# Optimization experiments

Hardware: AMD Instinct MI355X
Metric: run time of the kernel (lower is better)

Reference implementation:

```python
import jax, jax.numpy as jnp
import numpy as np
import math

D_MODEL = 2048
D_STATE = 64
D_CONV = 4
EXPAND = 2
HEADDIM = 128
NGROUPS = 1
CHUNK = 256
D_INNER = EXPAND * D_MODEL            # 4096
NHEADS = D_INNER // HEADDIM           # 32
CONV_DIM = D_INNER + 2 * NGROUPS * D_STATE   # 4224
D_IN_PROJ = 2 * D_INNER + 2 * NGROUPS * D_STATE + NHEADS  # 8352
BATCH, SEQLEN = 2, 4096
EPS = 1e-5


def segsum(x):
    # x: (..., T) -> (..., T, T) with s[i, j] = sum_{k=j+1}^{i} x[k], -inf above diag
    T = x.shape[-1]
    xx = jnp.broadcast_to(x[..., :, None], x.shape + (T,))
    mask_lo = jnp.tril(jnp.ones((T, T), dtype=bool), -1)
    xx = jnp.where(mask_lo, xx, 0.0)
    s = jnp.cumsum(xx, axis=-2)
    mask = jnp.tril(jnp.ones((T, T), dtype=bool), 0)
    return jnp.where(mask, s, -jnp.inf)


def ssd(X, A, B, C, block_len):
    # X:(b,L,h,p)  A:(b,L,h)  B,C:(b,L,h,n)
    b, L, h, p = X.shape
    c = L // block_len
    X = X.reshape(b, c, block_len, h, p)
    A = A.reshape(b, c, block_len, h).transpose(0, 3, 1, 2)  # b h c l
    B = B.reshape(b, c, block_len, h, -1)
    C = C.reshape(b, c, block_len, h, -1)
    A_cumsum = jnp.cumsum(A, axis=-1)
    Lmat = jnp.exp(segsum(A))                                  # b h c l l
    Y_diag = jnp.einsum('bclhn,bcshn,bhcls,bcshp->bclhp', C, B, Lmat, X)
    decay_states = jnp.exp(A_cumsum[:, :, :, -1:] - A_cumsum)  # b h c l
    states = jnp.einsum('bclhn,bhcl,bclhp->bchpn', B, decay_states, X)
    init = jnp.zeros_like(states[:, :1])
    states = jnp.concatenate([init, states], axis=1)
    decay_chunk = jnp.exp(segsum(jnp.pad(A_cumsum[:, :, :, -1], ((0, 0), (0, 0), (1, 0)))))
    new_states = jnp.einsum('bhzc,bchpn->bzhpn', decay_chunk, states)
    states, final_state = new_states[:, :-1], new_states[:, -1]
    Y_off = jnp.einsum('bclhn,bchpn,bhcl->bclhp', C, states, jnp.exp(A_cumsum))
    Y = (Y_diag + Y_off).reshape(b, L, h, p)
    return Y, final_state


def causal_dwconv(x, w, b):
    # x:(B,L,C)  w:(C,K) depthwise kernel  b:(C,)  -> causal conv, length preserved
    C, K = w.shape
    y = jax.lax.conv_general_dilated(
        x.transpose(0, 2, 1), w[:, None, :], (1,), [(K - 1, 0)],
        feature_group_count=C)
    return y.transpose(0, 2, 1) + b


def setup_inputs() -> dict:
    key = jax.random.key(0)
    ks = jax.random.split(key, 8)
    u = jax.random.normal(ks[0], (BATCH, SEQLEN, D_MODEL), dtype=jnp.float32)
    W_in = jax.random.normal(ks[1], (D_MODEL, D_IN_PROJ), dtype=jnp.float32) / np.sqrt(D_MODEL)
    conv_w = jax.random.normal(ks[2], (CONV_DIM, D_CONV), dtype=jnp.float32) / np.sqrt(D_CONV)
    conv_b = jnp.zeros((CONV_DIM,), dtype=jnp.float32)
    # dt_bias init: inverse-softplus of dt sampled log-uniform in [dt_min, dt_max]
    dt_min, dt_max, dt_floor = 1e-3, 1e-1, 1e-4
    dt = jnp.exp(jax.random.uniform(ks[3], (NHEADS,)) * (math.log(dt_max) - math.log(dt_min)) + math.log(dt_min))
    dt = jnp.clip(dt, dt_floor)
    dt_bias = dt + jnp.log(-jnp.expm1(-dt))
    A_log = jnp.log(jax.random.uniform(ks[4], (NHEADS,), minval=1.0, maxval=16.0))
    D = jnp.ones((NHEADS,), dtype=jnp.float32)
    norm_w = jnp.ones((D_INNER,), dtype=jnp.float32)
    W_out = jax.random.normal(ks[5], (D_INNER, D_MODEL), dtype=jnp.float32) / np.sqrt(D_INNER)
    return {"u": u, "W_in": W_in, "conv_w": conv_w, "conv_b": conv_b,
            "dt_bias": dt_bias, "A_log": A_log, "D": D, "norm_w": norm_w, "W_out": W_out}


def reference(u, W_in, conv_w, conv_b, dt_bias, A_log, D, norm_w, W_out):
    batch, seqlen, _ = u.shape
    zxbcdt = u @ W_in                                   # (B,L,8352)
    z, xBC, dt = jnp.split(zxbcdt, [D_INNER, D_INNER + CONV_DIM], axis=-1)
    dt = jax.nn.softplus(dt + dt_bias)                  # (B,L,H)
    xBC = jax.nn.silu(causal_dwconv(xBC, conv_w, conv_b))
    x, B, C = jnp.split(xBC, [D_INNER, D_INNER + NGROUPS * D_STATE], axis=-1)
    x = x.reshape(batch, seqlen, NHEADS, HEADDIM)
    B = jnp.broadcast_to(B.reshape(batch, seqlen, NGROUPS, D_STATE), (batch, seqlen, NHEADS, D_STATE))
    C = jnp.broadcast_to(C.reshape(batch, seqlen, NGROUPS, D_STATE), (batch, seqlen, NHEADS, D_STATE))
    A = -jnp.exp(A_log)                                 # (H,)
    x_scaled = x * dt[..., None]
    A_dt = A * dt                                       # (B,L,H)
    y, _final = ssd(x_scaled, A_dt, B, C, CHUNK)
    y = y.reshape(batch, seqlen, D_INNER)
    x_flat = x.reshape(batch, seqlen, D_INNER)
    D_full = jnp.repeat(D, HEADDIM)
    y = y + x_flat * D_full
    # gated RMSNorm, norm AFTER gate (norm_before_gate=False)
    yg = y * jax.nn.silu(z)
    var = jnp.mean(yg * yg, axis=-1, keepdims=True)
    y = yg * jax.lax.rsqrt(var + EPS) * norm_w
    return y @ W_out
```

## Files before the change

### kernel.cpp

```cpp
#include <hip/hip_runtime.h>

typedef short s8v __attribute__((ext_vector_type(8)));
typedef float f4v __attribute__((ext_vector_type(4)));
typedef unsigned short bfu;

#define MFMA16 __builtin_amdgcn_mfma_f32_16x16x32_bf16

constexpr int kSEQ = 4096;
constexpr int kBL  = 8192;
constexpr int kDM  = 2048;
constexpr int kDP  = 8352;
constexpr int kDPpad = 8448;
constexpr int kDI  = 4096;
constexpr int kCV  = 4224;
constexpr int kXBC = 4256;
constexpr int kNH  = 32;
constexpr int kHD  = 128;
constexpr int kDS  = 64;
constexpr int kCH  = 256;

#if defined(__has_builtin)
#  if __has_builtin(__builtin_amdgcn_global_load_lds)
#    define HAS_GLD 1
#  endif
#endif
#ifndef HAS_GLD
#  define HAS_GLD 0
#endif

__device__ __forceinline__ void gld_lds16(const void* g, void* lbase, int lane){
#if HAS_GLD
  (void)lane;
  __builtin_amdgcn_global_load_lds(
      (const __attribute__((address_space(1))) void*)g,
      (__attribute__((address_space(3))) void*)lbase, 16, 0, 0);
#else
  *(uint4*)((char*)lbase + lane * 16) = *(const uint4*)g;
#endif
}

__device__ __forceinline__ bfu f2bf(float f){
  union { float f; unsigned u; } c; c.f = f;
  return (bfu)((c.u + 0x7fffu + ((c.u >> 16) & 1u)) >> 16);
}
__device__ __forceinline__ float bf2f(bfu s){
  union { unsigned u; float f; } c; c.u = ((unsigned)s) << 16;
  return c.f;
}

__device__ __forceinline__ s8v frag_ld(const char* lds, int rowbase, int kh, int lane){
  int r = rowbase + (lane & 15);
  int slot = (kh << 2) + (lane >> 4);
  return *(const s8v*)(lds + (((r << 3) + (slot ^ (r & 7))) << 4));
}

__global__ __launch_bounds__(256) void k_zero(bfu* __restrict__ p, int n){
  int i = blockIdx.x * 256 + threadIdx.x;
  if (i < n) p[i] = 0;
}

__global__ __launch_bounds__(256) void k_cvt(const float* __restrict__ s, bfu* __restrict__ d, int n8){
  int i = blockIdx.x * 256 + threadIdx.x;
  int stride = gridDim.x * 256;
  for (; i < n8; i += stride){
    const float4* sp = (const float4*)(s + (size_t)i * 8);
    float4 a = sp[0], b = sp[1];
    uint4 pk; bfu* pp = (bfu*)&pk;
    pp[0]=f2bf(a.x); pp[1]=f2bf(a.y); pp[2]=f2bf(a.z); pp[3]=f2bf(a.w);
    pp[4]=f2bf(b.x); pp[5]=f2bf(b.y); pp[6]=f2bf(b.z); pp[7]=f2bf(b.w);
    *(uint4*)(d + (size_t)i * 8) = pk;
  }
}

__global__ __launch_bounds__(256) void k_transpose(const float* __restrict__ src, bfu* __restrict__ dst,
                                                   int R, int C, const float* __restrict__ scale){
  __shared__ float tile[32][33];
  int c0 = blockIdx.x * 32, r0 = blockIdx.y * 32;
  int tx = threadIdx.x, ty = threadIdx.y;
  #pragma unroll
  for (int i = ty; i < 32; i += 8){
    int r = r0 + i, cc = c0 + tx;
    tile[i][tx] = (r < R && cc < C) ? src[(size_t)r * C + cc] : 0.f;
  }
  __syncthreads();
  #pragma unroll
  for (int i = ty; i < 32; i += 8){
    int dr = c0 + i, dc = r0 + tx;
    if (dr < C && dc < R){
      float v = tile[tx][i];
      if (scale) v *= scale[dc];
      dst[(size_t)dr * R + dc] = f2bf(v);
    }
  }
}

template<int MODE>
__global__ __launch_bounds__(512, 2) void k_gemm256(const bfu* __restrict__ A, const bfu* __restrict__ Bt,
                                                    float* __restrict__ outF, bfu* __restrict__ outZ,
                                                    bfu* __restrict__ outX, const float* __restrict__ rsv,
                                                    int tilesN, int N, int K){
  extern __shared__ char lds[];
  int t = threadIdx.x, lane = t & 63, wave = t >> 6;
  int wr = wave >> 2, wc = wave & 3;
  int nwg = gridDim.x;
  int bid = blockIdx.x;
  int cpx = nwg >> 3;
  int wg = (bid & 7) * cpx + (bid >> 3);
  int tmTile = wg / tilesN, tnTile = wg % tilesN;
  int tm = tmTile << 8, tn = tnTile << 8;
  const bfu* Ab = A + (size_t)tm * K;
  const bfu* Bb = Bt + (size_t)tn * K;

  #define AU(b,kh) ((b) * 65536 + (kh) * 16384)
  #define BU(b,kh) ((b) * 65536 + 32768 + (kh) * 16384)

  auto stage_unit = [&](const bfu* srcbase, int unitOfs, int kcol0){
    #pragma unroll
    for (int j = 0; j < 2; ++j){
      int lg = j * 512 + wave * 64 + lane;
      int r = lg >> 2;
      int s = (lg & 3) ^ ((r >> 1) & 3);
      gld_lds16(srcbase + (size_t)r * K + kcol0 + s * 8,
                lds + unitOfs + (j * 512 + wave * 64) * 16, lane);
    }
  };
  auto rd_frag = [&](int unitOfs, int rbase) -> s8v {
    int r = rbase + (lane & 15);
    int s = lane >> 4;
    int g = (r << 2) + (s ^ ((r >> 1) & 3));
    return *(const s8v*)(lds + unitOfs + (g << 4));
  };

  f4v acc[8][4];
  f4v zz = {0.f, 0.f, 0.f, 0.f};
  #pragma unroll
  for (int m = 0; m < 8; ++m)
    #pragma unroll
    for (int n = 0; n < 4; ++n) acc[m][n] = zz;

  int nt = K >> 6;
  stage_unit(Ab, AU(0,0), 0);
  stage_unit(Bb, BU(0,0), 0);
  stage_unit(Ab, AU(0,1), 32);
  stage_unit(Bb, BU(0,1), 32);
  __builtin_amdgcn_sched_barrier(0);
  asm volatile("s_waitcnt vmcnt(4)" ::: "memory");
  __builtin_amdgcn_sched_barrier(0);
  __builtin_amdgcn_s_barrier();
  __builtin_amdgcn_sched_barrier(0);

  #pragma unroll 1
  for (int tt = 0; tt < nt; ++tt){
    int cb = tt & 1, nb = cb ^ 1;
    int k0n = (tt + 1) << 6;
    bool more = (tt + 1 < nt);
    #pragma unroll
    for (int kh = 0; kh < 2; ++kh){
      if (more){
        stage_unit(Ab, AU(nb,kh), k0n + kh * 32);
        stage_unit(Bb, BU(nb,kh), k0n + kh * 32);
      }
      s8v af[8], bf[4];
      #pragma unroll
      for (int m = 0; m < 8; ++m) af[m] = rd_frag(AU(cb,kh), wr * 128 + m * 16);
      #pragma unroll
      for (int n = 0; n < 4; ++n) bf[n] = rd_frag(BU(cb,kh), wc * 64 + n * 16);
      __builtin_amdgcn_s_setprio(1);
      #pragma unroll
      for (int n = 0; n < 4; ++n)
        #pragma unroll
        for (int m = 0; m < 8; ++m)
          acc[m][n] = MFMA16(af[m], bf[n], acc[m][n], 0, 0, 0);
      __builtin_amdgcn_s_setprio(0);
      __builtin_amdgcn_sched_barrier(0);
      if (more) { asm volatile("s_waitcnt vmcnt(4)" ::: "memory"); }
      else      { asm volatile("s_waitcnt vmcnt(0)" ::: "memory"); }
      __builtin_amdgcn_sched_barrier(0);
      __builtin_amdgcn_s_barrier();
      __builtin_amdgcn_sched_barrier(0);
    }
  }

  int r0 = (lane >> 4) << 2;
  if (MODE == 0){
    float* rsl = (float*)lds;
    if (t < 256) rsl[t] = rsv[tm + t];
    __syncthreads();
    #pragma unroll
    for (int m = 0; m < 8; ++m)
      #pragma unroll
      for (int n = 0; n < 4; ++n)
        #pragma unroll
        for (int r = 0; r < 4; ++r){
          int rl = wr * 128 + m * 16 + r0 + r;
          size_t rg = (size_t)(tm + rl);
          int cg = tn + wc * 64 + n * 16 + (lane & 15);
          outF[rg * N + cg] = acc[m][n][r] * rsl[rl];
        }
  } else {
    #pragma unroll
    for (int m = 0; m < 8; ++m)
      #pragma unroll
      for (int n = 0; n < 4; ++n){
        int col = wc * 64 + n * 16 + (lane & 15);
        int cs = col >> 3, cl = col & 7;
        #pragma unroll
        for (int r = 0; r < 4; ++r){
          int row = wr * 128 + m * 16 + r0 + r;
          *(bfu*)(lds + row * 512 + ((cs ^ (row & 7)) << 4) + cl * 2) = f2bf(acc[m][n][r]);
        }
      }
    __syncthreads();
    bfu* op; int ldo, cofs;
    if (tn < 4096){ op = outZ; ldo = 4096; cofs = 0; }
    else          { op = outX; ldo = kXBC; cofs = 4096; }
    int row = t >> 1, half = t & 1;
    bfu* baseo = op + (size_t)(tm + row) * ldo + (tn - cofs) + half * 128;
    #pragma unroll
    for (int i = 0; i < 16; ++i){
      int cg = tn + half * 128 + i * 8;
      if (cg < kDP){
        uint4 v = *(const uint4*)(lds + row * 512 + (((half * 16 + i) ^ (row & 7)) << 4));
        *(uint4*)(baseo + i * 8) = v;
      }
    }
  }
  #undef AU
  #undef BU
}

__global__ __launch_bounds__(256) void k_conv(const bfu* __restrict__ xbc, const float* __restrict__ cw,
    const float* __restrict__ cb, bfu* __restrict__ xT,
    bfu* __restrict__ B16o, bfu* __restrict__ BTo, bfu* __restrict__ C16o){
  int cht = blockIdx.x;
  int lt = blockIdx.y;
  int b = lt >> 6;
  int l0 = (lt & 63) << 6;
  int t = threadIdx.x;
  __shared__ float w[256];
  __shared__ float bias[64];
  __shared__ bfu in16[67][66];
  __shared__ bfu out16[64][66];
  if (t < 64) bias[t] = cb[cht * 64 + t];
  w[t] = cw[cht * 256 + t];
  int chbase = cht * 64;
  for (int i = t; i < 67 * 64; i += 256){
    int rrow = i >> 6, cc = i & 63;
    int l = l0 + rrow - 3;
    bfu hv = 0;
    if (l >= 0) hv = xbc[((size_t)b * kSEQ + l) * kXBC + chbase + cc];
    in16[rrow][cc] = hv;
  }
  __syncthreads();
  for (int i = t; i < 4096; i += 256){
    int lr = i >> 6, cc = i & 63;
    float acc = bias[cc];
    #pragma unroll
    for (int j = 0; j < 4; ++j)
      acc += bf2f(in16[lr + j][cc]) * w[cc * 4 + j];
    float sv = acc / (1.f + __expf(-acc));
    out16[lr][cc] = f2bf(sv);
  }
  __syncthreads();
  if (chbase >= 4096){
    for (int i = t; i < 4096; i += 256){
      int lr = i >> 6, cc = i & 63;
      size_t row = (size_t)b * kSEQ + l0 + lr;
      int ch = chbase + cc;
      bfu v = out16[lr][cc];
      if (ch < 4096 + kDS) B16o[row * kDS + (ch - 4096)] = v;
      else                 C16o[row * kDS + (ch - 4096 - kDS)] = v;
    }
  }
  if (chbase < 4096 + kDS){
    for (int i = t; i < 4096; i += 256){
      int cc = i >> 6, lr = i & 63;
      int ch = chbase + cc;
      int lg = l0 + lr;
      bfu v = out16[lr][cc];
      if (ch < 4096){
        int hh = ch >> 7, p = ch & 127;
        xT[(((size_t)b * kNH + hh) * kHD + p) * kSEQ + lg] = v;
      } else if (ch < 4096 + kDS){
        BTo[((size_t)b * kDS + (ch - 4096)) * kSEQ + lg] = v;
      }
    }
  }
}

__global__ __launch_bounds__(256) void k_dtscan(const bfu* __restrict__ xbc, const float* __restrict__ dt_bias,
    const float* __restrict__ A_log, float* __restrict__ dtf, float* __restrict__ acum){
  int bi = blockIdx.x;
  int h = bi & 31, c = (bi >> 5) & 15, b = bi >> 9;
  int t = threadIdx.x;
  size_t row = (size_t)b * kSEQ + c * kCH + t;
  float draw = bf2f(xbc[row * kXBC + kCV + h]) + dt_bias[h];
  float dt = (draw > 20.f) ? draw : log1pf(__expf(draw));
  dtf[row * kNH + h] = dt;
  float dA = -__expf(A_log[h]) * dt;
  __shared__ float s[256];
  s[t] = dA;
  __syncthreads();
  #pragma unroll
  for (int off = 1; off < 256; off <<= 1){
    float v = (t >= off) ? s[t - off] : 0.f;
    __syncthreads();
    s[t] += v;
    __syncthreads();
  }
  acum[(size_t)bi * 256 + t] = s[t];
}

__global__ __launch_bounds__(256) void k_states(const bfu* __restrict__ xT, const bfu* __restrict__ BT,
    const float* __restrict__ dtf, const float* __restrict__ acum, bfu* __restrict__ states){
  int bi = blockIdx.x;
  int h = bi & 31, c = (bi >> 5) & 15, b = bi >> 9;
  int t = threadIdx.x, lane = t & 63, wave = t >> 6;
  int wr = wave >> 1, wc = wave & 1;
  __shared__ uint4 ldsX4[1024];
  __shared__ uint4 ldsB4[512];
  __shared__ float dsv[256];
  char* ldsX = (char*)ldsX4;
  char* ldsB = (char*)ldsB4;
  float Atot = acum[(size_t)bi * 256 + 255];
  {
    size_t row = (size_t)b * kSEQ + c * kCH + t;
    dsv[t] = dtf[row * kNH + h] * __expf(Atot - acum[(size_t)bi * 256 + t]);
  }
  f4v zz = {0.f, 0.f, 0.f, 0.f};
  f4v acc[4][2];
  #pragma unroll
  for (int m = 0; m < 4; ++m){ acc[m][0] = zz; acc[m][1] = zz; }
  const bfu* xTp = xT + ((size_t)b * kNH + h) * kHD * kSEQ + c * kCH;
  const bfu* BTp = BT + (size_t)b * kDS * kSEQ + c * kCH;
  __syncthreads();
  for (int kb = 0; kb < 4; ++kb){
    #pragma unroll
    for (int it = 0; it < 4; ++it){
      int s = it * 256 + t;
      int row = s >> 3;
      int srcslot = (s & 7) ^ (row & 7);
      gld_lds16(xTp + (size_t)row * kSEQ + kb * 64 + srcslot * 8,
                ldsX + it * 4096 + wave * 1024, lane);
    }
    #pragma unroll
    for (int it = 0; it < 2; ++it){
      int cidx = it * 256 + t;
      int row = cidx >> 3, slot = cidx & 7;
      uint4 v = *(const uint4*)(BTp + (size_t)row * kSEQ + kb * 64 + slot * 8);
      bfu* hp = (bfu*)&v;
      #pragma unroll
      for (int j = 0; j < 8; ++j)
        hp[j] = f2bf(bf2f(hp[j]) * dsv[kb * 64 + slot * 8 + j]);
      *(uint4*)(ldsB + (((row << 3) + (slot ^ (row & 7))) << 4)) = v;
    }
    __syncthreads();
    s8v af[4][2], bb[2][2];
    #pragma unroll
    for (int m = 0; m < 4; ++m){
      af[m][0] = frag_ld(ldsX, wr * 64 + m * 16, 0, lane);
      af[m][1] = frag_ld(ldsX, wr * 64 + m * 16, 1, lane);
    }
    #pragma unroll
    for (int nf = 0; nf < 2; ++nf){
      bb[nf][0] = frag_ld(ldsB, wc * 32 + nf * 16, 0, lane);
      bb[nf][1] = frag_ld(ldsB, wc * 32 + nf * 16, 1, lane);
    }
    #pragma unroll
    for (int kh = 0; kh < 2; ++kh)
      #pragma unroll
      for (int m = 0; m < 4; ++m)
        #pragma unroll
        for (int nf = 0; nf < 2; ++nf)
          acc[m][nf] = MFMA16(af[m][kh], bb[nf][kh], acc[m][nf], 0, 0, 0);
    __syncthreads();
  }
  bfu* sp = states + (size_t)bi * 8192;
  int r0 = (lane >> 4) << 2;
  #pragma unroll
  for (int m = 0; m < 4; ++m)
    #pragma unroll
    for (int nf = 0; nf < 2; ++nf)
      #pragma unroll
      for (int r = 0; r < 4; ++r){
        int p = wr * 64 + m * 16 + r0 + r;
        int n = wc * 32 + nf * 16 + (lane & 15);
        sp[p * 64 + n] = f2bf(acc[m][nf][r]);
      }
}

__global__ __launch_bounds__(256) void k_scan(bfu* __restrict__ st, const float* __restrict__ acum){
  int bh = blockIdx.x >> 2;
  int jg = blockIdx.x & 3;
  int b = bh >> 5, h = bh & 31;
  int t = threadIdx.x;
  float run[8];
  #pragma unroll
  for (int j = 0; j < 8; ++j) run[j] = 0.f;
  for (int c = 0; c < 16; ++c){
    size_t bi = (size_t)((b * 16 + c) * 32 + h);
    float eT = __expf(acum[bi * 256 + 255]);
    size_t base = bi * 8192 + (size_t)jg * 2048;
    #pragma unroll
    for (int j = 0; j < 8; ++j){
      size_t idx = base + j * 256 + t;
      float sl = bf2f(st[idx]);
      st[idx] = f2bf(run[j]);
      run[j] = run[j] * eT + sl;
    }
  }
}

__global__ __launch_bounds__(256) void k_y(
    const bfu* __restrict__ xT, const bfu* __restrict__ Bm, const bfu* __restrict__ Cm,
    const bfu* __restrict__ SIs, const float* __restrict__ dtf, const float* __restrict__ acum,
    const bfu* __restrict__ z16, const float* __restrict__ Dp,
    bfu* __restrict__ y16)
{
  int bi = blockIdx.x;
  int h = bi & 31, c = (bi >> 5) & 15, b = bi >> 9;
  int ph = blockIdx.y;
  int t = threadIdx.x, lane = t & 63, wave = t >> 6;
  int wl = wave << 6;
  __shared__ uint4 ldsP4[2048];
  __shared__ uint4 ldsT4[512];
  __shared__ float acumS[256];
  __shared__ float dtS[256];
  char* ldsP = ((char*)ldsP4) + (wave << 13);
  char* ldsT = (char*)ldsT4;
  size_t rowbase = (size_t)b * kSEQ + c * kCH;
  acumS[t] = acum[(size_t)bi * 256 + t];
  dtS[t] = dtf[(rowbase + t) * kNH + h];
  const bfu* SIp = SIs + (size_t)bi * 8192 + (size_t)ph * 4096;
  #pragma unroll
  for (int it = 0; it < 2; ++it){
    int cidx = it * 256 + t;
    int row = cidx >> 3, slot = cidx & 7;
    uint4 v = *(const uint4*)(SIp + row * 64 + slot * 8);
    *(uint4*)(ldsT + (((row << 3) + (slot ^ (row & 7))) << 4)) = v;
  }
  const bfu* Cp = Cm + rowbase * kDS;
  s8v cf[4][2];
  #pragma unroll
  for (int m = 0; m < 4; ++m){
    cf[m][0] = *(const s8v*)(Cp + (size_t)(wl + m * 16 + (lane & 15)) * kDS + ((lane >> 4) << 3));
    cf[m][1] = *(const s8v*)(Cp + (size_t)(wl + m * 16 + (lane & 15)) * kDS + 32 + ((lane >> 4) << 3));
  }
  __syncthreads();
  float Arow[16];
  #pragma unroll
  for (int m = 0; m < 4; ++m)
    #pragma unroll
    for (int r = 0; r < 4; ++r)
      Arow[m * 4 + r] = acumS[wl + m * 16 + ((lane >> 4) << 2) + r];
  f4v acc[4][4];
  {
    s8v bfo[4][2];
    #pragma unroll
    for (int pf = 0; pf < 4; ++pf){
      bfo[pf][0] = frag_ld(ldsT, pf << 4, 0, lane);
      bfo[pf][1] = frag_ld(ldsT, pf << 4, 1, lane);
    }
    f4v zz = {0.f, 0.f, 0.f, 0.f};
    #pragma unroll
    for (int m = 0; m < 4; ++m)
      #pragma unroll
      for (int pf = 0; pf < 4; ++pf){
        f4v v = zz;
        v = MFMA16(cf[m][0], bfo[pf][0], v, 0, 0, 0);
        v = MFMA16(cf[m][1], bfo[pf][1], v, 0, 0, 0);
        #pragma unroll
        for (int r = 0; r < 4; ++r) v[r] *= __expf(Arow[m * 4 + r]);
        acc[m][pf] = v;
      }
  }
  float Dh = Dp[h];
  const bfu* Bp = Bm + rowbase * kDS;
  const bfu* xTp = xT + (((size_t)b * kNH + h) * kHD + ph * 64) * kSEQ + c * kCH;
  #pragma unroll 1
  for (int sb = 0; sb < 4; ++sb){
    __syncthreads();
    #pragma unroll
    for (int it = 0; it < 2; ++it){
      int s = it * 256 + t;
      int row = s >> 3;
      int srcslot = (s & 7) ^ (row & 7);
      gld_lds16(xTp + (size_t)row * kSEQ + sb * 64 + srcslot * 8,
                ldsT + it * 4096 + wave * 1024, lane);
    }
    f4v sv[4][4];
    {
      s8v bsf[4][2];
      #pragma unroll
      for (int sf = 0; sf < 4; ++sf){
        bsf[sf][0] = *(const s8v*)(Bp + (size_t)(sb * 64 + sf * 16 + (lane & 15)) * kDS + ((lane >> 4) << 3));
        bsf[sf][1] = *(const s8v*)(Bp + (size_t)(sb * 64 + sf * 16 + (lane & 15)) * kDS + 32 + ((lane >> 4) << 3));
      }
      f4v zz = {0.f, 0.f, 0.f, 0.f};
      #pragma unroll
      for (int m = 0; m < 4; ++m)
        #pragma unroll
        for (int sf = 0; sf < 4; ++sf){
          f4v v = zz;
          v = MFMA16(cf[m][0], bsf[sf][0], v, 0, 0, 0);
          v = MFMA16(cf[m][1], bsf[sf][1], v, 0, 0, 0);
          sv[m][sf] = v;
        }
    }
    int scb = sb << 6;
    float As[4], dts_[4];
    #pragma unroll
    for (int sf = 0; sf < 4; ++sf){
      As[sf] = acumS[scb + sf * 16 + (lane & 15)];
      dts_[sf] = dtS[scb + sf * 16 + (lane & 15)];
    }
    #pragma unroll
    for (int m = 0; m < 4; ++m)
      #pragma unroll
      for (int sf = 0; sf < 4; ++sf)
        #pragma unroll
        for (int r = 0; r < 4; ++r){
          int rloc = m * 16 + ((lane >> 4) << 2) + r;
          int scl = sf * 16 + (lane & 15);
          int d = (wl + rloc) - (scb + scl);
          float pv = 0.f;
          if (d >= 0)
            pv = sv[m][sf][r] * __expf(Arow[m * 4 + r] - As[sf]) * dts_[sf];
          if (d == 0)
            pv += Dh;
          *(bfu*)(ldsP + rloc * 128 + ((((scl >> 3) ^ (rloc & 7)) << 3) + (scl & 7)) * 2) = f2bf(pv);
        }
    __syncthreads();
    s8v xb[4][2];
    #pragma unroll
    for (int pf = 0; pf < 4; ++pf){
      xb[pf][0] = frag_ld(ldsT, pf << 4, 0, lane);
      xb[pf][1] = frag_ld(ldsT, pf << 4, 1, lane);
    }
    #pragma unroll
    for (int m = 0; m < 4; ++m){
      s8v pa0 = frag_ld(ldsP, m << 4, 0, lane);
      s8v pa1 = frag_ld(ldsP, m << 4, 1, lane);
      #pragma unroll
      for (int pf = 0; pf < 4; ++pf){
        acc[m][pf] = MFMA16(pa0, xb[pf][0], acc[m][pf], 0, 0, 0);
        acc[m][pf] = MFMA16(pa1, xb[pf][1], acc[m][pf], 0, 0, 0);
      }
    }
  }
  __syncthreads();
  char* ldsY = (char*)ldsP4;
  #pragma unroll
  for (int m = 0; m < 4; ++m)
    #pragma unroll
    for (int pf = 0; pf < 4; ++pf)
      #pragma unroll
      for (int r = 0; r < 4; ++r){
        int rloc = wl + m * 16 + ((lane >> 4) << 2) + r;
        int col  = (pf << 4) + (lane & 15);
        *(bfu*)(ldsY + rloc * 128 + (((col >> 3) ^ (rloc & 7)) << 4) + (col & 7) * 2) = f2bf(acc[m][pf][r]);
      }
  __syncthreads();
  int cg0 = (h << 7) + (ph << 6);
  #pragma unroll
  for (int j = 0; j < 8; ++j){
    int idx = j * 256 + t;
    int row = idx >> 3, g = idx & 7;
    uint4 yv = *(const uint4*)(ldsY + row * 128 + ((g ^ (row & 7)) << 4));
    size_t rowg = rowbase + row;
    uint4 zv4 = *(const uint4*)(z16 + rowg * kDI + cg0 + g * 8);
    const bfu* yp = (const bfu*)&yv;
    const bfu* zp = (const bfu*)&zv4;
    uint4 out; bfu* op = (bfu*)&out;
    #pragma unroll
    for (int e = 0; e < 8; ++e){
      float zv = bf2f(zp[e]);
      float sg = zv / (1.f + __expf(-zv));
      op[e] = f2bf(bf2f(yp[e]) * sg);
    }
    *(uint4*)(y16 + rowg * kDI + cg0 + g * 8) = out;
  }
}

__global__ __launch_bounds__(256) void k_rms(const bfu* __restrict__ y, float* __restrict__ rs){
  int row = blockIdx.x;
  int t = threadIdx.x, lane = t & 63, wave = t >> 6;
  const bfu* yp = y + (size_t)row * kDI;
  uint4 a = *(const uint4*)(yp + t * 8);
  uint4 b = *(const uint4*)(yp + 2048 + t * 8);
  const bfu* ap = (const bfu*)&a;
  const bfu* bp = (const bfu*)&b;
  float ss = 0.f;
  #pragma unroll
  for (int j = 0; j < 8; ++j){
    float va = bf2f(ap[j]); ss += va * va;
    float vb = bf2f(bp[j]); ss += vb * vb;
  }
  #pragma unroll
  for (int o = 32; o > 0; o >>= 1) ss += __shfl_down(ss, o, 64);
  __shared__ float red[4];
  if (lane == 0) red[wave] = ss;
  __syncthreads();
  if (t == 0){
    float tot = red[0] + red[1] + red[2] + red[3];
    rs[row] = rsqrtf(tot * (1.f / 4096.f) + 1e-5f);
  }
}

extern "C" void kernel_launch(void* const* d_in, const int* in_sizes, int n_in,
                              void* d_out, int out_size, void* d_ws, size_t ws_size,
                              hipStream_t stream){
  (void)in_sizes; (void)n_in; (void)out_size; (void)ws_size;
  const float* u       = (const float*)d_in[0];
  const float* W_in    = (const float*)d_in[1];
  const float* conv_w  = (const float*)d_in[2];
  const float* conv_b  = (const float*)d_in[3];
  const float* dt_bias = (const float*)d_in[4];
  const float* A_log   = (const float*)d_in[5];
  const float* Dp      = (const float*)d_in[6];
  const float* norm_w  = (const float*)d_in[7];
  const float* W_out   = (const float*)d_in[8];
  char* ws = (char*)d_ws;

  const size_t o_z    = 0;
  const size_t o_xbc  = o_z   + (size_t)kBL * kDI * 2;
  const size_t o_u16  = o_xbc + (size_t)kBL * kXBC * 2;
  const size_t o_xT   = o_u16 + (size_t)kBL * kDM * 2;
  const size_t o_B16  = o_xT  + (size_t)kBL * kDI * 2;
  const size_t o_BT   = o_B16 + (size_t)kBL * kDS * 2;
  const size_t o_C16  = o_BT  + (size_t)kBL * kDS * 2;
  const size_t o_dtf  = o_C16 + (size_t)kBL * kDS * 2;
  const size_t o_acum = o_dtf + (size_t)kBL * kNH * 4;
  const size_t o_rs   = o_acum + (size_t)1024 * 256 * 4;
  const size_t o_states = o_u16;
  const size_t o_woutT  = o_u16 + (size_t)1024 * 8192 * 2;
  const size_t o_winT   = o_xT;
  const size_t o_y16    = o_xbc;

  bfu* z16    = (bfu*)(ws + o_z);
  bfu* xbc    = (bfu*)(ws + o_xbc);
  bfu* u16    = (bfu*)(ws + o_u16);
  bfu* xT     = (bfu*)(ws + o_xT);
  bfu* B16    = (bfu*)(ws + o_B16);
  bfu* BT     = (bfu*)(ws + o_BT);
  bfu* C16    = (bfu*)(ws + o_C16);
  float* dtf  = (float*)(ws + o_dtf);
  float* acum = (float*)(ws + o_acum);
  float* rs   = (float*)(ws + o_rs);
  bfu* statesS= (bfu*)(ws + o_states);
  bfu* woutT  = (bfu*)(ws + o_woutT);
  bfu* winT   = (bfu*)(ws + o_winT);
  bfu* y16    = (bfu*)(ws + o_y16);

  (void)hipFuncSetAttribute(reinterpret_cast<const void*>(&k_gemm256<2>),
                            hipFuncAttributeMaxDynamicSharedMemorySize, 131072);
  (void)hipFuncSetAttribute(reinterpret_cast<const void*>(&k_gemm256<0>),
                            hipFuncAttributeMaxDynamicSharedMemorySize, 131072);

  k_zero<<<(96 * kDM + 255) / 256, 256, 0, stream>>>(winT + (size_t)kDP * kDM, 96 * kDM);
  k_cvt<<<2048, 256, 0, stream>>>(u, u16, kBL * kDM / 8);
  k_transpose<<<dim3(kDP / 32, kDM / 32), dim3(32, 8), 0, stream>>>(W_in, winT, kDM, kDP, nullptr);
  k_gemm256<2><<<(kDPpad / 256) * (kBL / 256), 512, 131072, stream>>>(u16, winT, nullptr, z16, xbc, nullptr, kDPpad / 256, kDPpad, kDM);
  k_conv<<<dim3(kCV / 64, kBL / 64), 256, 0, stream>>>(xbc, conv_w, conv_b, xT, B16, BT, C16);
  k_dtscan<<<1024, 256, 0, stream>>>(xbc, dt_bias, A_log, dtf, acum);
  k_transpose<<<dim3(kDM / 32, kDI / 32), dim3(32, 8), 0, stream>>>(W_out, woutT, kDI, kDM, norm_w);
  k_states<<<1024, 256, 0, stream>>>(xT, BT, dtf, acum, statesS);
  k_scan<<<256, 256, 0, stream>>>(statesS, acum);
  k_y<<<dim3(1024, 2), 256, 0, stream>>>(xT, B16, C16, statesS, dtf, acum, z16, Dp, y16);
  k_rms<<<kBL, 256, 0, stream>>>(y16, rs);
  k_gemm256<0><<<(kDM / 256) * (kBL / 256), 512, 131072, stream>>>(y16, woutT, (float*)d_out, nullptr, nullptr, rs, kDM / 256, kDM, kDI);
}
```

Measured before the change: 858.7 us.

## Restructure GEMM main loop into 4-stage K=32 LDS pipeline with split phases

The 256x256 GEMM main loop now moves through K in 32-wide steps using a four-buffer LDS ring with three tiles prefetched ahead, replacing the earlier double-buffered 64-wide steps. Each step is split into two phases that each load half of the A fragments and issue half of the next global-to-LDS copies, interleaved with MFMA work. The XOR swizzle on LDS addresses is removed in favour of a plain row layout. The goal is to hide more global memory latency and spread LDS reads. The cost is more barriers per K step, and the unswizzled layout may cause LDS bank conflicts.

```diff
diff --git a/kernel.cpp b/kernel.cpp
--- a/kernel.cpp
+++ b/kernel.cpp
@@ -111,25 +111,13 @@
   const bfu* Ab = A + (size_t)tm * K;
   const bfu* Bb = Bt + (size_t)tn * K;
 
-  #define AU(b,kh) ((b) * 65536 + (kh) * 16384)
-  #define BU(b,kh) ((b) * 65536 + 32768 + (kh) * 16384)
-
-  auto stage_unit = [&](const bfu* srcbase, int unitOfs, int kcol0){
-    #pragma unroll
-    for (int j = 0; j < 2; ++j){
-      int lg = j * 512 + wave * 64 + lane;
-      int r = lg >> 2;
-      int s = (lg & 3) ^ ((r >> 1) & 3);
-      gld_lds16(srcbase + (size_t)r * K + kcol0 + s * 8,
-                lds + unitOfs + (j * 512 + wave * 64) * 16, lane);
-    }
+  int sr = t >> 2, scc = t & 3;
+  auto stage_half = [&](const bfu* src, int ldsOfs, int kcol0){
+    gld_lds16(src + (size_t)sr * K + kcol0 + scc * 8,
+              lds + ldsOfs + (wave << 10), lane);
   };
-  auto rd_frag = [&](int unitOfs, int rbase) -> s8v {
-    int r = rbase + (lane & 15);
-    int s = lane >> 4;
-    int g = (r << 2) + (s ^ ((r >> 1) & 3));
-    return *(const s8v*)(lds + unitOfs + (g << 4));
-  };
+  int aoff = ((wr * 128 + (lane & 15)) << 6) + ((lane >> 4) << 4);
+  int boff = 16384 + ((wc * 64 + (lane & 15)) << 6) + ((lane >> 4) << 4);
 
   f4v acc[8][4];
   f4v zz = {0.f, 0.f, 0.f, 0.f};
@@ -138,44 +126,66 @@
     #pragma unroll
     for (int n = 0; n < 4; ++n) acc[m][n] = zz;
 
-  int nt = K >> 6;
-  stage_unit(Ab, AU(0,0), 0);
-  stage_unit(Bb, BU(0,0), 0);
-  stage_unit(Ab, AU(0,1), 32);
-  stage_unit(Bb, BU(0,1), 32);
+  int nt = K >> 5;
+  #pragma unroll
+  for (int pt = 0; pt < 3; ++pt){
+    int bofs = pt * 32768, kc = pt << 5;
+    stage_half(Ab,                   bofs,         kc);
+    stage_half(Ab + (size_t)128 * K, bofs + 8192,  kc);
+    stage_half(Bb,                   bofs + 16384, kc);
+    stage_half(Bb + (size_t)128 * K, bofs + 24576, kc);
+  }
   __builtin_amdgcn_sched_barrier(0);
-  asm volatile("s_waitcnt vmcnt(4)" ::: "memory");
+  asm volatile("s_waitcnt vmcnt(8)" ::: "memory");
   __builtin_amdgcn_sched_barrier(0);
   __builtin_amdgcn_s_barrier();
   __builtin_amdgcn_sched_barrier(0);
 
   #pragma unroll 1
   for (int tt = 0; tt < nt; ++tt){
-    int cb = tt & 1, nb = cb ^ 1;
-    int k0n = (tt + 1) << 6;
-    bool more = (tt + 1 < nt);
-    #pragma unroll
-    for (int kh = 0; kh < 2; ++kh){
-      if (more){
-        stage_unit(Ab, AU(nb,kh), k0n + kh * 32);
-        stage_unit(Bb, BU(nb,kh), k0n + kh * 32);
-      }
-      s8v af[8], bf[4];
-      #pragma unroll
-      for (int m = 0; m < 8; ++m) af[m] = rd_frag(AU(cb,kh), wr * 128 + m * 16);
-      #pragma unroll
-      for (int n = 0; n < 4; ++n) bf[n] = rd_frag(BU(cb,kh), wc * 64 + n * 16);
+    int cb = (tt & 3) * 32768;
+    int tn3 = tt + 3;
+    bool st = tn3 < nt;
+    int b3 = (tn3 & 3) * 32768, kc3 = tn3 << 5;
+    s8v bf[4];
+    #pragma unroll
+    for (int ph = 0; ph < 2; ++ph){
+      s8v af[4];
+      #pragma unroll
+      for (int i = 0; i < 4; ++i)
+        af[i] = *(const s8v*)(lds + cb + aoff + ((ph * 64 + i * 16) << 6));
+      if (ph == 0){
+        #pragma unroll
+        for (int j = 0; j < 4; ++j)
+          bf[j] = *(const s8v*)(lds + cb + boff + ((j * 16) << 6));
+      }
+      if (st){
+        if (ph == 0){
+          stage_half(Ab,                   b3,        kc3);
+          stage_half(Ab + (size_t)128 * K, b3 + 8192, kc3);
+        } else {
+          stage_half(Bb,                   b3 + 16384, kc3);
+          stage_half(Bb + (size_t)128 * K, b3 + 24576, kc3);
+        }
+      }
+      __builtin_amdgcn_sched_barrier(0);
+      __builtin_amdgcn_s_barrier();
+      asm volatile("s_waitcnt lgkmcnt(0)" ::: "memory");
+      __builtin_amdgcn_sched_barrier(0);
       __builtin_amdgcn_s_setprio(1);
       #pragma unroll
       for (int n = 0; n < 4; ++n)
         #pragma unroll
-        for (int m = 0; m < 8; ++m)
-          acc[m][n] = MFMA16(af[m], bf[n], acc[m][n], 0, 0, 0);
+        for (int i = 0; i < 4; ++i)
+          acc[ph * 4 + i][n] = MFMA16(af[i], bf[n], acc[ph * 4 + i][n], 0, 0, 0);
       __builtin_amdgcn_s_setprio(0);
       __builtin_amdgcn_sched_barrier(0);
-      if (more) { asm volatile("s_waitcnt vmcnt(4)" ::: "memory"); }
-      else      { asm volatile("s_waitcnt vmcnt(0)" ::: "memory"); }
-      __builtin_amdgcn_sched_barrier(0);
+      if (ph == 1){
+        if (tt < nt - 3)      { asm volatile("s_waitcnt vmcnt(8)" ::: "memory"); }
+        else if (tt == nt - 3){ asm volatile("s_waitcnt vmcnt(4)" ::: "memory"); }
+        else                  { asm volatile("s_waitcnt vmcnt(0)" ::: "memory"); }
+        __builtin_amdgcn_sched_barrier(0);
+      }
       __builtin_amdgcn_s_barrier();
       __builtin_amdgcn_sched_barrier(0);
     }
@@ -225,8 +235,6 @@
       }
     }
   }
-  #undef AU
-  #undef BU
 }
 
 __global__ __launch_bounds__(256) void k_conv(const bfu* __restrict__ xbc, const float* __restrict__ cw,
```

Result: slower. 878.4 us (+2.3%).
